# Kernel optimization log

Hardware: AMD Instinct MI355X
Metric: run time of the kernel (lower is better)

Reference implementation:

```python
import jax, jax.numpy as jnp
import numpy as np

EPS = 1e-3  # keras LayerNormalization default epsilon


def _ln(x, g, b):
    m = jnp.mean(x, axis=-1, keepdims=True)
    v = jnp.mean(jnp.square(x - m), axis=-1, keepdims=True)
    return (x - m) * jax.lax.rsqrt(v + EPS) * g + b


def setup_inputs() -> dict:
    key = jax.random.key(0)
    B, T, C, H = 64, 256, 1024, 16
    D = C // H
    ks = jax.random.split(key, 16)
    s = 0.02
    return {
        "x": jax.random.normal(ks[0], (B, T, C), jnp.float32),
        # per-head q/k/v projections (no bias), stacked over heads [H, C, D]
        "wq": jax.random.normal(ks[1], (H, C, D), jnp.float32) * s,
        "wk": jax.random.normal(ks[2], (H, C, D), jnp.float32) * s,
        "wv": jax.random.normal(ks[3], (H, C, D), jnp.float32) * s,
        "w_proj": jax.random.normal(ks[4], (C, C), jnp.float32) * s,
        "b_proj": jnp.zeros((C,), jnp.float32),
        # FFN: C -> 4C (relu) -> C
        "w1": jax.random.normal(ks[5], (C, 4 * C), jnp.float32) * s,
        "b1": jnp.zeros((4 * C,), jnp.float32),
        "w2": jax.random.normal(ks[6], (4 * C, C), jnp.float32) * s,
        "b2": jnp.zeros((C,), jnp.float32),
        # LayerNorm params: ln1 (pre-attn), ln2 (pre-ffn), ln3 (inside FeedForward)
        "g1": jnp.ones((C,), jnp.float32), "be1": jnp.zeros((C,), jnp.float32),
        "g2": jnp.ones((C,), jnp.float32), "be2": jnp.zeros((C,), jnp.float32),
        "g3": jnp.ones((C,), jnp.float32), "be3": jnp.zeros((C,), jnp.float32),
    }


def reference(x, wq, wk, wv, w_proj, b_proj, w1, b1, w2, b2,
              g1, be1, g2, be2, g3, be3):
    B, T, C = x.shape
    # --- multi-head causal self-attention on LN1(x) ---
    h = _ln(x, g1, be1)
    q = jnp.einsum('btc,hcd->bhtd', h, wq)
    k = jnp.einsum('btc,hcd->bhtd', h, wk)
    v = jnp.einsum('btc,hcd->bhtd', h, wv)
    # NOTE: original scales by C**-0.5 with C = n_embd (full dim), not head_size
    scores = jnp.einsum('bhtd,bhsd->bhts', q, k) * (C ** -0.5)
    causal = jnp.tril(jnp.ones((T, T), dtype=bool))
    scores = jnp.where(causal, scores, -jnp.inf)
    attn = jax.nn.softmax(scores, axis=-1)  # dropout is identity at inference
    out = jnp.einsum('bhts,bhsd->bhtd', attn, v)
    out = out.transpose(0, 2, 1, 3).reshape(B, T, C)  # concat heads
    out = out @ w_proj + b_proj
    x = x + out
    # --- FeedForward block (contains its own residual + LayerNorm) ---
    y = _ln(x, g2, be2)
    z = jax.nn.relu(y @ w1 + b1) @ w2 + b2
    return x + _ln(y + z, g3, be3)
```

## Files before the change

kernel.cpp:

```cpp
#include <hip/hip_runtime.h>

typedef __bf16 bf16_t;
typedef __bf16 bf16x8 __attribute__((ext_vector_type(8)));
typedef float f32x4 __attribute__((ext_vector_type(4)));

#define LN_EPS 1e-3f

__device__ __forceinline__ void gload_lds16(const void* g, void* l) {
    __builtin_amdgcn_global_load_lds(
        (__attribute__((address_space(1))) void*)(g),
        (__attribute__((address_space(3))) void*)(l), 16, 0, 0);
}

__global__ __launch_bounds__(256)
void transpose_f32_bf16(const float* __restrict__ in, bf16_t* __restrict__ outp,
                        int ldi, int ldo)
{
    __shared__ float tile[64][65];
    const int k0 = blockIdx.x * 64, n0 = blockIdx.y * 64;
    const int tid = threadIdx.x;
    const int r = tid >> 2;
    const int q = tid & 3;
    const float* src = in + (long)(k0 + r) * ldi + n0 + q * 16;
#pragma unroll
    for (int j = 0; j < 4; ++j) {
        float4 v = *(const float4*)(src + j * 4);
        tile[r][q * 16 + j * 4 + 0] = v.x;
        tile[r][q * 16 + j * 4 + 1] = v.y;
        tile[r][q * 16 + j * 4 + 2] = v.z;
        tile[r][q * 16 + j * 4 + 3] = v.w;
    }
    __syncthreads();
    union { bf16_t e[16]; uint4 u[2]; } pk;
#pragma unroll
    for (int j = 0; j < 16; ++j) pk.e[j] = (bf16_t)tile[q * 16 + j][r];
    bf16_t* dst = outp + (long)(n0 + r) * ldo + k0 + q * 16;
    *(uint4*)(dst)     = pk.u[0];
    *(uint4*)(dst + 8) = pk.u[1];
}

__global__ __launch_bounds__(256)
void pack_qkv_t(const float* __restrict__ wq, const float* __restrict__ wk,
                const float* __restrict__ wv, bf16_t* __restrict__ outp)
{
    __shared__ float tile[64][65];
    const int m   = blockIdx.y;
    const int sel = m >> 4, h = m & 15;
    const float* in = ((sel == 0) ? wq : (sel == 1) ? wk : wv) + (long)h * 65536;
    bf16_t* out = outp + ((long)sel * 1024 + h * 64) * 1024;
    const int k0 = blockIdx.x * 64;
    const int tid = threadIdx.x;
    const int r = tid >> 2;
    const int q = tid & 3;
    const float* src = in + (long)(k0 + r) * 64 + q * 16;
#pragma unroll
    for (int j = 0; j < 4; ++j) {
        float4 v = *(const float4*)(src + j * 4);
        tile[r][q * 16 + j * 4 + 0] = v.x;
        tile[r][q * 16 + j * 4 + 1] = v.y;
        tile[r][q * 16 + j * 4 + 2] = v.z;
        tile[r][q * 16 + j * 4 + 3] = v.w;
    }
    __syncthreads();
    union { bf16_t e[16]; uint4 u[2]; } pk;
#pragma unroll
    for (int j = 0; j < 16; ++j) pk.e[j] = (bf16_t)tile[q * 16 + j][r];
    bf16_t* dst = out + (long)r * 1024 + k0 + q * 16;
    *(uint4*)(dst)     = pk.u[0];
    *(uint4*)(dst + 8) = pk.u[1];
}

__global__ __launch_bounds__(256)
void v_transpose(const bf16_t* __restrict__ qkv, bf16_t* __restrict__ vt)
{
    int g  = blockIdx.x * 256 + threadIdx.x;
    int bh = g >> 11;
    int r  = g & 2047;
    int d  = r & 63;
    int sg = r >> 6;
    int b  = bh >> 4, h = bh & 15;
    const bf16_t* src = qkv + ((long)b * 256 + sg * 8) * 3072 + 2048 + h * 64 + d;
    union { bf16_t e[8]; uint4 u; } pk;
#pragma unroll
    for (int e = 0; e < 8; ++e) pk.e[e] = src[(long)e * 3072];
    *(uint4*)(vt + ((long)bh * 64 + d) * 256 + sg * 8) = pk.u;
}

__global__ __launch_bounds__(256)
void ln_fwd(const float* __restrict__ in, const float* __restrict__ g,
            const float* __restrict__ be, bf16_t* __restrict__ outp)
{
    const long row = blockIdx.x;
    const int t = threadIdx.x;
    float4 v = ((const float4*)(in + row * 1024))[t];
    float s  = v.x + v.y + v.z + v.w;
    float sq = v.x * v.x + v.y * v.y + v.z * v.z + v.w * v.w;
#pragma unroll
    for (int off = 1; off < 64; off <<= 1) {
        s  += __shfl_xor(s, off);
        sq += __shfl_xor(sq, off);
    }
    __shared__ float red[8];
    if ((t & 63) == 0) { red[(t >> 6) * 2] = s; red[(t >> 6) * 2 + 1] = sq; }
    __syncthreads();
    s  = red[0] + red[2] + red[4] + red[6];
    sq = red[1] + red[3] + red[5] + red[7];
    float mean = s * 0.0009765625f;
    float var  = sq * 0.0009765625f - mean * mean;
    float rstd = rsqrtf(var + LN_EPS);
    float4 gv = ((const float4*)g)[t];
    float4 bv = ((const float4*)be)[t];
    union { bf16_t h[4]; uint2 u; } pk;
    pk.h[0] = (bf16_t)((v.x - mean) * rstd * gv.x + bv.x);
    pk.h[1] = (bf16_t)((v.y - mean) * rstd * gv.y + bv.y);
    pk.h[2] = (bf16_t)((v.z - mean) * rstd * gv.z + bv.z);
    pk.h[3] = (bf16_t)((v.w - mean) * rstd * gv.w + bv.w);
    *(uint2*)(outp + row * 1024 + t * 4) = pk.u;
}

__global__ __launch_bounds__(256)
void ln3_kernel(const bf16_t* __restrict__ in, const float* __restrict__ g,
                const float* __restrict__ be, float* outp, const float* res)
{
    const long row = blockIdx.x;
    const int t = threadIdx.x;
    union { uint2 u; bf16_t h[4]; } pk;
    pk.u = *(const uint2*)(in + row * 1024 + t * 4);
    float v0 = (float)pk.h[0], v1 = (float)pk.h[1], v2 = (float)pk.h[2], v3 = (float)pk.h[3];
    float s  = v0 + v1 + v2 + v3;
    float sq = v0 * v0 + v1 * v1 + v2 * v2 + v3 * v3;
#pragma unroll
    for (int off = 1; off < 64; off <<= 1) {
        s  += __shfl_xor(s, off);
        sq += __shfl_xor(sq, off);
    }
    __shared__ float red[8];
    if ((t & 63) == 0) { red[(t >> 6) * 2] = s; red[(t >> 6) * 2 + 1] = sq; }
    __syncthreads();
    s  = red[0] + red[2] + red[4] + red[6];
    sq = red[1] + red[3] + red[5] + red[7];
    float mean = s * 0.0009765625f;
    float var  = sq * 0.0009765625f - mean * mean;
    float rstd = rsqrtf(var + LN_EPS);
    float4 gv = ((const float4*)g)[t];
    float4 bv = ((const float4*)be)[t];
    float4 rv = ((const float4*)(res + row * 1024))[t];
    float4 ov;
    ov.x = rv.x + (v0 - mean) * rstd * gv.x + bv.x;
    ov.y = rv.y + (v1 - mean) * rstd * gv.y + bv.y;
    ov.z = rv.z + (v2 - mean) * rstd * gv.z + bv.z;
    ov.w = rv.w + (v3 - mean) * rstd * gv.w + bv.w;
    ((float4*)outp)[row * 256 + t] = ov;
}

template<int MODE>
__global__ __launch_bounds__(512, 2)
void gemm_bt(const bf16_t* __restrict__ Ap, const bf16_t* __restrict__ Bp,
             void* outp, const float* __restrict__ bias,
             const void* addp, int M, int N, int K)
{
    __shared__ __attribute__((aligned(16))) bf16_t As0[256 * 64];
    __shared__ __attribute__((aligned(16))) bf16_t As1[256 * 64];
    __shared__ __attribute__((aligned(16))) bf16_t As2[256 * 64];
    __shared__ __attribute__((aligned(16))) bf16_t Bs0[256 * 64];
    __shared__ __attribute__((aligned(16))) bf16_t Bs1[256 * 64];

    const int tid  = threadIdx.x;
    const int w    = tid >> 6, lane = tid & 63;
    const int l16  = lane & 15, lg = lane >> 4;
    const int wm   = w >> 2, wn = w & 3;
    const int srow = lane >> 3;
    const int sslot = lane & 7;

    const int gx  = gridDim.x;
    const int gy  = gridDim.y;
    const int nwg = gx * gy;
    const int bid = blockIdx.y * gx + blockIdx.x;
    const int cpx = nwg >> 3;
    const int sid = (bid & 7) * cpx + (bid >> 3);
    const long m0 = (long)(sid / gy) * 256;
    const long n0 = (long)(sid % gy) * 256;
    const int nkt = K >> 6;

    f32x4 acc[8][4] = {};
    bf16x8 a[4][2], b0[2][2], b1[2][2];

    auto STAGEH = [&](const bf16_t* src, long row0, int kt, bf16_t* dst, int h) {
#pragma unroll
        for (int i = 0; i < 2; ++i) {
            int r  = h * 128 + w * 16 + i * 8 + srow;
            int ss = sslot ^ (r & 7);
            gload_lds16(src + (row0 + r) * (long)K + (long)kt * 64 + ss * 8,
                        dst + (h * 128 + w * 16 + i * 8) * 64);
        }
    };

#define LDA_M(buf, mh) do {                                               \
    _Pragma("unroll") for (int j = 0; j < 4; ++j)                         \
    _Pragma("unroll") for (int kk = 0; kk < 2; ++kk) {                    \
        int r  = wm * 128 + (mh) * 64 + j * 16 + l16;                     \
        int ss = (kk * 4 + lg) ^ (r & 7);                                 \
        a[j][kk] = *(const bf16x8*)&buf[r * 64 + ss * 8];                 \
    } } while (0)

#define LDB_M(dst, buf, nh) do {                                          \
    _Pragma("unroll") for (int n = 0; n < 2; ++n)                         \
    _Pragma("unroll") for (int kk = 0; kk < 2; ++kk) {                    \
        int r  = wn * 64 + ((nh) * 2 + n) * 16 + l16;                     \
        int ss = (kk * 4 + lg) ^ (r & 7);                                 \
        dst[n][kk] = *(const bf16x8*)&buf[r * 64 + ss * 8];               \
    } } while (0)

#define MMA_M(bv, mh, nh) do {                                            \
    __builtin_amdgcn_s_setprio(1);                                        \
    _Pragma("unroll") for (int j = 0; j < 4; ++j)                         \
    _Pragma("unroll") for (int n = 0; n < 2; ++n)                         \
    _Pragma("unroll") for (int kk = 0; kk < 2; ++kk)                      \
        acc[(mh) * 4 + j][(nh) * 2 + n] =                                 \
            __builtin_amdgcn_mfma_f32_16x16x32_bf16(                      \
                a[j][kk], bv[n][kk], acc[(mh) * 4 + j][(nh) * 2 + n],     \
                0, 0, 0);                                                 \
    __builtin_amdgcn_s_setprio(0);                                        \
} while (0)

#define PRE_MFMA() do { __builtin_amdgcn_s_barrier();                     \
    asm volatile("s_waitcnt lgkmcnt(0)" ::: "memory");                    \
    __builtin_amdgcn_sched_barrier(0); } while (0)

    STAGEH(Ap, m0, 0, As0, 0); STAGEH(Ap, m0, 0, As0, 1);
    STAGEH(Bp, n0, 0, Bs0, 0); STAGEH(Bp, n0, 0, Bs0, 1);
    STAGEH(Ap, m0, 1, As1, 0); STAGEH(Ap, m0, 1, As1, 1);
    asm volatile("s_waitcnt vmcnt(0)" ::: "memory");
    __builtin_amdgcn_s_barrier();
    __builtin_amdgcn_sched_barrier(0);

    bf16_t *Ar = As0, *An1 = As1, *An2 = As2;
    bf16_t *Br = Bs0, *Bw = Bs1;

    for (int c = 0; c < nkt; ++c) {
        const bool pfa = (c + 2 < nkt);
        const bool pfb = (c + 1 < nkt);

        LDA_M(Ar, 0); LDB_M(b0, Br, 0);
        if (pfb) { STAGEH(Bp, n0, c + 1, Bw, 0); STAGEH(Bp, n0, c + 1, Bw, 1); }
        if (pfa) STAGEH(Ap, m0, c + 2, An2, 0);
        PRE_MFMA(); MMA_M(b0, 0, 0); __builtin_amdgcn_s_barrier();
        LDB_M(b1, Br, 1);
        PRE_MFMA(); MMA_M(b1, 0, 1); __builtin_amdgcn_s_barrier();
        LDA_M(Ar, 1);
        if (pfa) STAGEH(Ap, m0, c + 2, An2, 1);
        PRE_MFMA(); MMA_M(b1, 1, 1); __builtin_amdgcn_s_barrier();
        if (pfa) { asm volatile("s_waitcnt vmcnt(4)" ::: "memory"); }
        else     { asm volatile("s_waitcnt vmcnt(0)" ::: "memory"); }
        __builtin_amdgcn_s_barrier();
        __builtin_amdgcn_sched_barrier(0);
        MMA_M(b0, 1, 0); __builtin_amdgcn_s_barrier();

        bf16_t* t = Ar; Ar = An1; An1 = An2; An2 = t;
        t = Br; Br = Bw; Bw = t;
    }

#pragma unroll
    for (int fm = 0; fm < 8; ++fm) {
#pragma unroll
        for (int fn = 0; fn < 4; ++fn) {
            const long gcol = n0 + wn * 64 + fn * 16 + l16;
            float bv = 0.f;
            if (MODE != 0) bv = bias[gcol];
#pragma unroll
            for (int e = 0; e < 4; ++e) {
                const long grow = m0 + wm * 128 + fm * 16 + lg * 4 + e;
                float v = acc[fm][fn][e];
                if (MODE == 0) {
                    ((bf16_t*)outp)[grow * N + gcol] = (bf16_t)v;
                } else if (MODE == 1) {
                    v += bv + ((const float*)addp)[grow * N + gcol];
                    ((float*)outp)[grow * N + gcol] = v;
                } else if (MODE == 2) {
                    v += bv; v = v > 0.f ? v : 0.f;
                    ((bf16_t*)outp)[grow * N + gcol] = (bf16_t)v;
                } else {
                    v += bv + (float)((const bf16_t*)addp)[grow * N + gcol];
                    ((bf16_t*)outp)[grow * N + gcol] = (bf16_t)v;
                }
            }
        }
    }
#undef LDA_M
#undef LDB_M
#undef MMA_M
#undef PRE_MFMA
}

__global__ __launch_bounds__(256)
void attn_kernel(const bf16_t* __restrict__ qkv, const bf16_t* __restrict__ vt,
                 bf16_t* __restrict__ outp)
{
    __shared__ __attribute__((aligned(16))) bf16_t Kt[64 * 64];
    __shared__ __attribute__((aligned(16))) bf16_t Vt[64 * 64];
    __shared__ __attribute__((aligned(16))) bf16_t Ps[4][16 * 72];

    const int tid = threadIdx.x, w = tid >> 6, lane = tid & 63;
    const int l16 = lane & 15, lg = lane >> 4;
    const int b = blockIdx.x >> 4, hh = blockIdx.x & 15;
    const bf16_t* pq = qkv + (long)(b * 256) * 3072 + hh * 64;
    const bf16_t* pv = vt + (long)blockIdx.x * 64 * 256;
    const int sr8 = lane >> 3;
    const int sl  = lane & 7;

    bf16x8 qf[4][2];
#pragma unroll
    for (int fm = 0; fm < 4; ++fm)
#pragma unroll
        for (int kk = 0; kk < 2; ++kk)
            qf[fm][kk] = *(const bf16x8*)(pq + (long)(w * 64 + fm * 16 + l16) * 3072
                                          + kk * 32 + lg * 8);

    f32x4 o[4][4] = {};
    float mrun[4][4], lrun[4][4];
#pragma unroll
    for (int i = 0; i < 4; ++i)
#pragma unroll
        for (int j = 0; j < 4; ++j) { mrun[i][j] = -__builtin_inff(); lrun[i][j] = 0.f; }

    for (int st = 0; st < 4; ++st) {
        __syncthreads();
#pragma unroll
        for (int i = 0; i < 2; ++i) {
            int r  = w * 16 + i * 8 + sr8;
            int ss = sl ^ (r & 7);
            gload_lds16(pq + (long)(st * 64 + r) * 3072 + 1024 + ss * 8,
                        &Kt[(w * 16 + i * 8) * 64]);
            gload_lds16(pv + (long)r * 256 + st * 64 + ss * 8,
                        &Vt[(w * 16 + i * 8) * 64]);
        }
        asm volatile("s_waitcnt vmcnt(0)" ::: "memory");
        __syncthreads();
        if (st > w) continue;

        f32x4 s[4][4] = {};
#pragma unroll
        for (int ks = 0; ks < 2; ++ks) {
            bf16x8 kb[4];
#pragma unroll
            for (int fs = 0; fs < 4; ++fs)
                kb[fs] = *(const bf16x8*)&Kt[(fs * 16 + l16) * 64
                                             + ((ks * 4 + lg) ^ (l16 & 7)) * 8];
#pragma unroll
            for (int fm = 0; fm < 4; ++fm)
#pragma unroll
                for (int fs = 0; fs < 4; ++fs)
                    s[fm][fs] = __builtin_amdgcn_mfma_f32_16x16x32_bf16(
                        qf[fm][ks], kb[fs], s[fm][fs], 0, 0, 0);
        }

#pragma unroll
        for (int fm = 0; fm < 4; ++fm) {
#pragma unroll
            for (int fs = 0; fs < 4; ++fs)
#pragma unroll
                for (int e = 0; e < 4; ++e) {
                    float v = s[fm][fs][e] * 0.03125f;
                    if (st == w && (fs * 16 + l16) > (fm * 16 + lg * 4 + e))
                        v = -__builtin_inff();
                    s[fm][fs][e] = v;
                }
#pragma unroll
            for (int e = 0; e < 4; ++e) {
                float pm = fmaxf(fmaxf(s[fm][0][e], s[fm][1][e]),
                                 fmaxf(s[fm][2][e], s[fm][3][e]));
#pragma unroll
                for (int off = 1; off < 16; off <<= 1) pm = fmaxf(pm, __shfl_xor(pm, off));
                float mnew  = fmaxf(mrun[fm][e], pm);
                float alpha = __expf(mrun[fm][e] - mnew);
                float rs = 0.f;
#pragma unroll
                for (int fs = 0; fs < 4; ++fs) {
                    float p = __expf(s[fm][fs][e] - mnew);
                    s[fm][fs][e] = p;
                    rs += p;
                }
#pragma unroll
                for (int off = 1; off < 16; off <<= 1) rs += __shfl_xor(rs, off);
                lrun[fm][e] = lrun[fm][e] * alpha + rs;
                mrun[fm][e] = mnew;
#pragma unroll
                for (int fd = 0; fd < 4; ++fd) o[fm][fd][e] *= alpha;
            }
#pragma unroll
            for (int fs = 0; fs < 4; ++fs)
#pragma unroll
                for (int e = 0; e < 4; ++e)
                    Ps[w][(lg * 4 + e) * 72 + fs * 16 + l16] = (bf16_t)s[fm][fs][e];
            bf16x8 ap0 = *(const bf16x8*)&Ps[w][l16 * 72 + lg * 8];
            bf16x8 ap1 = *(const bf16x8*)&Ps[w][l16 * 72 + 32 + lg * 8];
#pragma unroll
            for (int fd = 0; fd < 4; ++fd) {
                bf16x8 vb0 = *(const bf16x8*)&Vt[(fd * 16 + l16) * 64
                                                 + ((lg) ^ (l16 & 7)) * 8];
                bf16x8 vb1 = *(const bf16x8*)&Vt[(fd * 16 + l16) * 64
                                                 + ((4 + lg) ^ (l16 & 7)) * 8];
                o[fm][fd] = __builtin_amdgcn_mfma_f32_16x16x32_bf16(ap0, vb0, o[fm][fd], 0, 0, 0);
                o[fm][fd] = __builtin_amdgcn_mfma_f32_16x16x32_bf16(ap1, vb1, o[fm][fd], 0, 0, 0);
            }
        }
    }

#pragma unroll
    for (int fm = 0; fm < 4; ++fm)
#pragma unroll
        for (int e = 0; e < 4; ++e) {
            float inv = 1.f / lrun[fm][e];
            long row = (long)b * 256 + w * 64 + fm * 16 + lg * 4 + e;
#pragma unroll
            for (int fd = 0; fd < 4; ++fd)
                outp[row * 1024 + hh * 64 + fd * 16 + l16] =
                    (bf16_t)(o[fm][fd][e] * inv);
        }
}

extern "C" void kernel_launch(void* const* d_in, const int* in_sizes, int n_in,
                              void* d_out, int out_size, void* d_ws, size_t ws_size,
                              hipStream_t stream)
{
    (void)in_sizes; (void)n_in; (void)out_size; (void)ws_size;
    const float* x      = (const float*)d_in[0];
    const float* wq     = (const float*)d_in[1];
    const float* wk     = (const float*)d_in[2];
    const float* wv     = (const float*)d_in[3];
    const float* w_proj = (const float*)d_in[4];
    const float* b_proj = (const float*)d_in[5];
    const float* w1     = (const float*)d_in[6];
    const float* b1     = (const float*)d_in[7];
    const float* w2     = (const float*)d_in[8];
    const float* b2     = (const float*)d_in[9];
    const float* g1  = (const float*)d_in[10]; const float* be1 = (const float*)d_in[11];
    const float* g2  = (const float*)d_in[12]; const float* be2 = (const float*)d_in[13];
    const float* g3  = (const float*)d_in[14]; const float* be3 = (const float*)d_in[15];

    char* ws = (char*)d_ws;
    bf16_t* wqkv  = (bf16_t*)(ws + 0);
    bf16_t* wproj = (bf16_t*)(ws + 6291456);
    bf16_t* w1t   = (bf16_t*)(ws + 8388608);
    bf16_t* w2t   = (bf16_t*)(ws + 16777216);
    bf16_t* h     = (bf16_t*)(ws + 25165824);
    bf16_t* qkv   = (bf16_t*)(ws + 58720256);
    bf16_t* attn  = h;
    bf16_t* u     = h;
    bf16_t* y     = (bf16_t*)(ws + 159383552);
    bf16_t* vt    = y;
    float*  x2    = (float*)d_out;
    bf16_t* tbuf  = y;

    const int M = 16384;

    transpose_f32_bf16<<<dim3(16, 16), 256, 0, stream>>>(w_proj, wproj, 1024, 1024);
    transpose_f32_bf16<<<dim3(16, 64), 256, 0, stream>>>(w1, w1t, 4096, 1024);
    transpose_f32_bf16<<<dim3(64, 16), 256, 0, stream>>>(w2, w2t, 1024, 4096);
    pack_qkv_t<<<dim3(16, 48), 256, 0, stream>>>(wq, wk, wv, wqkv);

    ln_fwd<<<M, 256, 0, stream>>>(x, g1, be1, h);
    gemm_bt<0><<<dim3(64, 12), 512, 0, stream>>>(h, wqkv, qkv, nullptr, nullptr, M, 3072, 1024);
    v_transpose<<<8192, 256, 0, stream>>>(qkv, vt);
    attn_kernel<<<1024, 256, 0, stream>>>(qkv, vt, attn);
    gemm_bt<1><<<dim3(64, 4), 512, 0, stream>>>(attn, wproj, x2, b_proj, x, M, 1024, 1024);
    ln_fwd<<<M, 256, 0, stream>>>(x2, g2, be2, y);
    gemm_bt<2><<<dim3(64, 16), 512, 0, stream>>>(y, w1t, u, b1, nullptr, M, 4096, 1024);
    gemm_bt<3><<<dim3(64, 4), 512, 0, stream>>>(u, w2t, tbuf, b2, y, M, 1024, 4096);
    ln3_kernel<<<M, 256, 0, stream>>>(tbuf, g3, be3, (float*)d_out, x2);
}
```

Baseline: 655.4 us.

## Fuse V transpose into QKV GEMM epilogue and rebalance attention work

The QKV GEMM gains a mode that writes the V columns straight into a transposed per-head layout, so the separate v_transpose kernel and its extra pass over V are removed. The attention kernel now interleaves query rows across waves (row = fm*64 + w*16) so every wave does a similar amount of causal work instead of wave 3 doing four times as much as wave 0. It also double-buffers the K/V LDS tiles so the next tile loads while the current one is computed. The V stores in the epilogue are 8-byte strided writes, which may coalesce less well than the row-major output.

Result: faster. 634.6 us (-3.2%).

```diff
diff --git a/kernel.cpp b/kernel.cpp
--- a/kernel.cpp
+++ b/kernel.cpp
@@ -68,22 +68,6 @@
     bf16_t* dst = out + (long)r * 1024 + k0 + q * 16;
     *(uint4*)(dst)     = pk.u[0];
     *(uint4*)(dst + 8) = pk.u[1];
-}
-
-__global__ __launch_bounds__(256)
-void v_transpose(const bf16_t* __restrict__ qkv, bf16_t* __restrict__ vt)
-{
-    int g  = blockIdx.x * 256 + threadIdx.x;
-    int bh = g >> 11;
-    int r  = g & 2047;
-    int d  = r & 63;
-    int sg = r >> 6;
-    int b  = bh >> 4, h = bh & 15;
-    const bf16_t* src = qkv + ((long)b * 256 + sg * 8) * 3072 + 2048 + h * 64 + d;
-    union { bf16_t e[8]; uint4 u; } pk;
-#pragma unroll
-    for (int e = 0; e < 8; ++e) pk.e[e] = src[(long)e * 3072];
-    *(uint4*)(vt + ((long)bh * 64 + d) * 256 + sg * 8) = pk.u;
 }
 
 __global__ __launch_bounds__(256)
@@ -266,12 +250,24 @@
         for (int fn = 0; fn < 4; ++fn) {
             const long gcol = n0 + wn * 64 + fn * 16 + l16;
             float bv = 0.f;
-            if (MODE != 0) bv = bias[gcol];
+            if (MODE != 0 && MODE != 4) bv = bias[gcol];
+            const long grow0 = m0 + wm * 128 + fm * 16 + lg * 4;
+            if (MODE == 4 && gcol >= 2048) {
+                union { bf16_t h[4]; uint2 u; } pk;
+#pragma unroll
+                for (int e = 0; e < 4; ++e) pk.h[e] = (bf16_t)acc[fm][fn][e];
+                const int hh = (int)(gcol >> 6) - 32;
+                const int d  = (int)gcol & 63;
+                const long bb = grow0 >> 8;
+                const int s0  = (int)grow0 & 255;
+                *(uint2*)((bf16_t*)addp + ((bb * 16 + hh) * 64 + d) * 256 + s0) = pk.u;
+                continue;
+            }
 #pragma unroll
             for (int e = 0; e < 4; ++e) {
-                const long grow = m0 + wm * 128 + fm * 16 + lg * 4 + e;
+                const long grow = grow0 + e;
                 float v = acc[fm][fn][e];
-                if (MODE == 0) {
+                if (MODE == 0 || MODE == 4) {
                     ((bf16_t*)outp)[grow * N + gcol] = (bf16_t)v;
                 } else if (MODE == 1) {
                     v += bv + ((const float*)addp)[grow * N + gcol];
@@ -296,8 +292,8 @@
 void attn_kernel(const bf16_t* __restrict__ qkv, const bf16_t* __restrict__ vt,
                  bf16_t* __restrict__ outp)
 {
-    __shared__ __attribute__((aligned(16))) bf16_t Kt[64 * 64];
-    __shared__ __attribute__((aligned(16))) bf16_t Vt[64 * 64];
+    __shared__ __attribute__((aligned(16))) bf16_t Kt[2][64 * 64];
+    __shared__ __attribute__((aligned(16))) bf16_t Vt[2][64 * 64];
     __shared__ __attribute__((aligned(16))) bf16_t Ps[4][16 * 72];
 
     const int tid = threadIdx.x, w = tid >> 6, lane = tid & 63;
@@ -313,7 +309,7 @@
     for (int fm = 0; fm < 4; ++fm)
 #pragma unroll
         for (int kk = 0; kk < 2; ++kk)
-            qf[fm][kk] = *(const bf16x8*)(pq + (long)(w * 64 + fm * 16 + l16) * 3072
+            qf[fm][kk] = *(const bf16x8*)(pq + (long)(fm * 64 + w * 16 + l16) * 3072
                                           + kk * 32 + lg * 8);
 
     f32x4 o[4][4] = {};
@@ -323,20 +319,26 @@
 #pragma unroll
         for (int j = 0; j < 4; ++j) { mrun[i][j] = -__builtin_inff(); lrun[i][j] = 0.f; }
 
-    for (int st = 0; st < 4; ++st) {
-        __syncthreads();
+    auto STAGE = [&](int st, int bb) {
 #pragma unroll
         for (int i = 0; i < 2; ++i) {
             int r  = w * 16 + i * 8 + sr8;
             int ss = sl ^ (r & 7);
             gload_lds16(pq + (long)(st * 64 + r) * 3072 + 1024 + ss * 8,
-                        &Kt[(w * 16 + i * 8) * 64]);
+                        &Kt[bb][(w * 16 + i * 8) * 64]);
             gload_lds16(pv + (long)r * 256 + st * 64 + ss * 8,
-                        &Vt[(w * 16 + i * 8) * 64]);
-        }
-        asm volatile("s_waitcnt vmcnt(0)" ::: "memory");
-        __syncthreads();
-        if (st > w) continue;
+                        &Vt[bb][(w * 16 + i * 8) * 64]);
+        }
+    };
+
+    STAGE(0, 0);
+    asm volatile("s_waitcnt vmcnt(0)" ::: "memory");
+    __syncthreads();
+
+#pragma unroll
+    for (int st = 0; st < 4; ++st) {
+        const int cb = st & 1;
+        if (st < 3) STAGE(st + 1, cb ^ 1);
 
         f32x4 s[4][4] = {};
 #pragma unroll
@@ -344,24 +346,27 @@
             bf16x8 kb[4];
 #pragma unroll
             for (int fs = 0; fs < 4; ++fs)
-                kb[fs] = *(const bf16x8*)&Kt[(fs * 16 + l16) * 64
-                                             + ((ks * 4 + lg) ^ (l16 & 7)) * 8];
-#pragma unroll
-            for (int fm = 0; fm < 4; ++fm)
+                kb[fs] = *(const bf16x8*)&Kt[cb][(fs * 16 + l16) * 64
+                                               + ((ks * 4 + lg) ^ (l16 & 7)) * 8];
+#pragma unroll
+            for (int fm = 0; fm < 4; ++fm) {
+                if (fm < st) continue;
 #pragma unroll
                 for (int fs = 0; fs < 4; ++fs)
                     s[fm][fs] = __builtin_amdgcn_mfma_f32_16x16x32_bf16(
                         qf[fm][ks], kb[fs], s[fm][fs], 0, 0, 0);
+            }
         }
 
 #pragma unroll
         for (int fm = 0; fm < 4; ++fm) {
+            if (fm < st) continue;
 #pragma unroll
             for (int fs = 0; fs < 4; ++fs)
 #pragma unroll
                 for (int e = 0; e < 4; ++e) {
                     float v = s[fm][fs][e] * 0.03125f;
-                    if (st == w && (fs * 16 + l16) > (fm * 16 + lg * 4 + e))
+                    if (st == fm && (fs * 16 + l16) > (w * 16 + lg * 4 + e))
                         v = -__builtin_inff();
                     s[fm][fs][e] = v;
                 }
@@ -396,14 +401,16 @@
             bf16x8 ap1 = *(const bf16x8*)&Ps[w][l16 * 72 + 32 + lg * 8];
 #pragma unroll
             for (int fd = 0; fd < 4; ++fd) {
-                bf16x8 vb0 = *(const bf16x8*)&Vt[(fd * 16 + l16) * 64
-                                                 + ((lg) ^ (l16 & 7)) * 8];
-                bf16x8 vb1 = *(const bf16x8*)&Vt[(fd * 16 + l16) * 64
-                                                 + ((4 + lg) ^ (l16 & 7)) * 8];
+                bf16x8 vb0 = *(const bf16x8*)&Vt[cb][(fd * 16 + l16) * 64
+                                                    + ((lg) ^ (l16 & 7)) * 8];
+                bf16x8 vb1 = *(const bf16x8*)&Vt[cb][(fd * 16 + l16) * 64
+                                                    + ((4 + lg) ^ (l16 & 7)) * 8];
                 o[fm][fd] = __builtin_amdgcn_mfma_f32_16x16x32_bf16(ap0, vb0, o[fm][fd], 0, 0, 0);
                 o[fm][fd] = __builtin_amdgcn_mfma_f32_16x16x32_bf16(ap1, vb1, o[fm][fd], 0, 0, 0);
             }
         }
+        asm volatile("s_waitcnt vmcnt(0)" ::: "memory");
+        __syncthreads();
     }
 
 #pragma unroll
@@ -411,7 +418,7 @@
 #pragma unroll
         for (int e = 0; e < 4; ++e) {
             float inv = 1.f / lrun[fm][e];
-            long row = (long)b * 256 + w * 64 + fm * 16 + lg * 4 + e;
+            long row = (long)b * 256 + fm * 64 + w * 16 + lg * 4 + e;
 #pragma unroll
             for (int fd = 0; fd < 4; ++fd)
                 outp[row * 1024 + hh * 64 + fd * 16 + l16] =
@@ -460,8 +467,7 @@
     pack_qkv_t<<<dim3(16, 48), 256, 0, stream>>>(wq, wk, wv, wqkv);
 
     ln_fwd<<<M, 256, 0, stream>>>(x, g1, be1, h);
-    gemm_bt<0><<<dim3(64, 12), 512, 0, stream>>>(h, wqkv, qkv, nullptr, nullptr, M, 3072, 1024);
-    v_transpose<<<8192, 256, 0, stream>>>(qkv, vt);
+    gemm_bt<4><<<dim3(64, 12), 512, 0, stream>>>(h, wqkv, qkv, nullptr, vt, M, 3072, 1024);
     attn_kernel<<<1024, 256, 0, stream>>>(qkv, vt, attn);
     gemm_bt<1><<<dim3(64, 4), 512, 0, stream>>>(attn, wproj, x2, b_proj, x, M, 1024, 1024);
     ln_fwd<<<M, 256, 0, stream>>>(x2, g2, be2, y);
```
